# Performance work log

Measured on AMD Instinct MI355X. Metric: run time of the kernel, lower is better.

The kernel has to match this reference:

```python
import jax, jax.numpy as jnp
import numpy as np

EMBED = 1024
HEADS = 16
HEAD_DIM = EMBED // HEADS


def setup_inputs() -> dict:
    key = jax.random.key(0)
    ks = jax.random.split(key, 6)
    scale = 1.0 / np.sqrt(EMBED)
    x = jax.random.normal(ks[0], (2, 2048, EMBED), dtype=jnp.float32)
    # nn.Linear weights stored as [out_features, in_features]
    Wq = jax.random.normal(ks[1], (EMBED, EMBED), dtype=jnp.float32) * scale
    Wk = jax.random.normal(ks[2], (EMBED, EMBED), dtype=jnp.float32) * scale
    Wv = jax.random.normal(ks[3], (EMBED, EMBED), dtype=jnp.float32) * scale
    Wo = jax.random.normal(ks[4], (EMBED, EMBED), dtype=jnp.float32) * scale
    bo = jax.random.normal(ks[5], (EMBED,), dtype=jnp.float32) * scale
    return {"x": x, "Wq": Wq, "Wk": Wk, "Wv": Wv, "Wo": Wo, "bo": bo}


def reference(x, Wq, Wk, Wv, Wo, bo):
    N, L, E = x.shape
    # projections (torch Linear: x @ W.T)
    q = (x @ Wq.T).reshape(N, L, HEADS, HEAD_DIM).transpose(0, 2, 1, 3)  # [N,H,L,D]
    k = (x @ Wk.T).reshape(N, L, HEADS, HEAD_DIM).transpose(0, 2, 1, 3)
    v = (x @ Wv.T).reshape(N, L, HEADS, HEAD_DIM).transpose(0, 2, 1, 3)
    # scores scaled by sqrt(embed_size) (as in source, not sqrt(head_dim))
    scores = jnp.einsum("nhqd,nhkd->nhqk", q, k) / jnp.sqrt(jnp.float32(E))
    attn = jax.nn.softmax(scores, axis=-1)
    out = jnp.einsum("nhqk,nhkd->nhqd", attn, v)  # [N,H,L,D]
    out = out.transpose(0, 2, 1, 3).reshape(N, L, E)
    return out @ Wo.T + bo
```

## Files before the change

### kernel.cpp

```cpp
#include <hip/hip_runtime.h>
#include <hip/hip_bf16.h>

constexpr int NB  = 2;
constexpr int SL  = 2048;
constexpr int EMB = 1024;
constexpr int NH  = 16;
constexpr int HD  = 64;
constexpr int MT  = NB * SL;
constexpr size_t PROJ = (size_t)MT * EMB;

typedef __attribute__((ext_vector_type(8))) short bf16x8;
typedef __attribute__((ext_vector_type(4))) float f32x4;

__device__ inline short f2b(float f) {
  __hip_bfloat16 b = __float2bfloat16(f);
  short s; __builtin_memcpy(&s, &b, 2); return s;
}

#define GLDS16(g, l)                                                     \
  __builtin_amdgcn_global_load_lds(                                      \
      (const __attribute__((address_space(1))) void*)(g),                \
      (__attribute__((address_space(3))) void*)(l), 16, 0, 0)

__global__ __launch_bounds__(256) void cast_all(
    const float* __restrict__ x,  const float* __restrict__ wq,
    const float* __restrict__ wk, const float* __restrict__ wv,
    const float* __restrict__ wo, short* __restrict__ xb,
    short* __restrict__ wqkv, short* __restrict__ wob) {
  const size_t t = (size_t)blockIdx.x * 256 + threadIdx.x;
  const float* src; short* dst; size_t base;
  if (t < 1048576)      { src = x;  dst = xb;              base = 0; }
  else if (t < 1310720) { src = wq; dst = wqkv;            base = 1048576; }
  else if (t < 1572864) { src = wk; dst = wqkv + (1 << 20); base = 1310720; }
  else if (t < 1835008) { src = wv; dst = wqkv + (2 << 20); base = 1572864; }
  else                  { src = wo; dst = wob;             base = 1835008; }
  const size_t i = t - base;
  const float4 v = ((const float4*)src)[i];
  const short4 o = {f2b(v.x), f2b(v.y), f2b(v.z), f2b(v.w)};
  ((short4*)dst)[i] = o;
}

__global__ __launch_bounds__(256) void gemm_qkv(
    const short* __restrict__ A, const short* __restrict__ W,
    short* __restrict__ qb, short* __restrict__ kb, short* __restrict__ vt) {
  __shared__ short As[128 * 32];
  __shared__ short Bs[128 * 32];
  const int tid = threadIdx.x;
  const int w = tid >> 6, lane = tid & 63;
  const int la = lane >> 4, lb = lane & 15;
  const int wm = w & 1, wn = w >> 1;
  const int m0 = blockIdx.y << 7, n0 = blockIdx.x << 7;
  const int srow = lane >> 2, scol = (lane & 3) << 3;
  const short* a0 = A + (size_t)(m0 + w * 16 + srow) * 1024 + scol;
  const short* b0 = W + (size_t)(n0 + w * 16 + srow) * 1024 + scol;
  short* lA0 = As + (w * 16) * 32;
  short* lA1 = As + (64 + w * 16) * 32;
  short* lB0 = Bs + (w * 16) * 32;
  short* lB1 = Bs + (64 + w * 16) * 32;

  f32x4 acc[4][4];
#pragma unroll
  for (int i = 0; i < 4; ++i)
#pragma unroll
    for (int j = 0; j < 4; ++j) acc[i][j] = (f32x4){0.f, 0.f, 0.f, 0.f};

  for (int k0 = 0; k0 < 1024; k0 += 32) {
    __syncthreads();
    GLDS16(a0 + k0, lA0);
    GLDS16(a0 + 64 * 1024 + k0, lA1);
    GLDS16(b0 + k0, lB0);
    GLDS16(b0 + 64 * 1024 + k0, lB1);
    __syncthreads();
    bf16x8 af[4], bf[4];
#pragma unroll
    for (int i = 0; i < 4; ++i)
      af[i] = *(const bf16x8*)&As[(wm * 64 + i * 16 + lb) * 32 + la * 8];
#pragma unroll
    for (int j = 0; j < 4; ++j)
      bf[j] = *(const bf16x8*)&Bs[(wn * 64 + j * 16 + lb) * 32 + la * 8];
#pragma unroll
    for (int i = 0; i < 4; ++i)
#pragma unroll
      for (int j = 0; j < 4; ++j)
        acc[i][j] = __builtin_amdgcn_mfma_f32_16x16x32_bf16(af[i], bf[j],
                                                            acc[i][j], 0, 0, 0);
  }

  const int region = n0 >> 10;
  if (region < 2) {
    short* dst = region ? kb : qb;
    const float sc = region ? 1.0f : 0.03125f * 1.44269504f;
    const int nb0 = n0 & 1023;
#pragma unroll
    for (int j = 0; j < 4; ++j) {
      const int nj = nb0 + wn * 64 + j * 16 + lb;
#pragma unroll
      for (int i = 0; i < 4; ++i) {
        const int mi = m0 + wm * 64 + i * 16 + la * 4;
#pragma unroll
        for (int r = 0; r < 4; ++r)
          dst[(size_t)(mi + r) * 1024 + nj] = f2b(acc[i][j][r] * sc);
      }
    }
  } else {
#pragma unroll
    for (int j = 0; j < 4; ++j) {
      const int nv = (n0 - 2048) + wn * 64 + j * 16 + lb;
      const int h = nv >> 6, d = nv & 63;
#pragma unroll
      for (int i = 0; i < 4; ++i) {
        const int mi = m0 + wm * 64 + i * 16 + la * 4;
        const int nbi = mi >> 11, seq = mi & (SL - 1);
        const int k5 = seq & 31;
        const int seqp = (seq & ~31) | (8 * ((k5 >> 2) & 3) + 4 * (k5 >> 4));
        const short4 o = {f2b(acc[i][j][0]), f2b(acc[i][j][1]),
                          f2b(acc[i][j][2]), f2b(acc[i][j][3])};
        *(short4*)&vt[((size_t)(nbi * NH + h) * HD + d) * SL + seqp] = o;
      }
    }
  }
}

__global__ __launch_bounds__(256) void gemm_out(
    const short* __restrict__ A, const short* __restrict__ W,
    const float* __restrict__ bias, float* __restrict__ out) {
  __shared__ short As[128 * 32];
  __shared__ short Bs[64 * 32];
  const int tid = threadIdx.x;
  const int w = tid >> 6, lane = tid & 63;
  const int la = lane >> 4, lb = lane & 15;
  const int wm = w & 1, wn = w >> 1;
  const int m0 = blockIdx.y << 7, n0 = blockIdx.x << 6;
  const int srow = lane >> 2, scol = (lane & 3) << 3;
  const short* a0 = A + (size_t)(m0 + w * 16 + srow) * 1024 + scol;
  const short* b0 = W + (size_t)(n0 + w * 16 + srow) * 1024 + scol;
  short* lA0 = As + (w * 16) * 32;
  short* lA1 = As + (64 + w * 16) * 32;
  short* lB0 = Bs + (w * 16) * 32;

  f32x4 acc[4][2];
#pragma unroll
  for (int i = 0; i < 4; ++i)
#pragma unroll
    for (int j = 0; j < 2; ++j) acc[i][j] = (f32x4){0.f, 0.f, 0.f, 0.f};

  for (int k0 = 0; k0 < 1024; k0 += 32) {
    __syncthreads();
    GLDS16(a0 + k0, lA0);
    GLDS16(a0 + 64 * 1024 + k0, lA1);
    GLDS16(b0 + k0, lB0);
    __syncthreads();
    bf16x8 af[4], bf[2];
#pragma unroll
    for (int i = 0; i < 4; ++i)
      af[i] = *(const bf16x8*)&As[(wm * 64 + i * 16 + lb) * 32 + la * 8];
#pragma unroll
    for (int j = 0; j < 2; ++j)
      bf[j] = *(const bf16x8*)&Bs[(wn * 32 + j * 16 + lb) * 32 + la * 8];
#pragma unroll
    for (int i = 0; i < 4; ++i)
#pragma unroll
      for (int j = 0; j < 2; ++j)
        acc[i][j] = __builtin_amdgcn_mfma_f32_16x16x32_bf16(af[i], bf[j],
                                                            acc[i][j], 0, 0, 0);
  }
#pragma unroll
  for (int j = 0; j < 2; ++j) {
    const int nj = n0 + wn * 32 + j * 16 + lb;
    const float bv = bias[nj];
#pragma unroll
    for (int i = 0; i < 4; ++i) {
      const int mi = m0 + wm * 64 + i * 16 + la * 4;
#pragma unroll
      for (int r = 0; r < 4; ++r)
        out[(size_t)(mi + r) * 1024 + nj] = acc[i][j][r] + bv;
    }
  }
}

__global__ __launch_bounds__(256, 2) void attn_mfma(const short* __restrict__ Qg,
                                                    const short* __restrict__ Kg,
                                                    const short* __restrict__ Vtg,
                                                    short* __restrict__ Ab) {
  __shared__ __align__(16) short mem[17408];
  __shared__ float lred[128];
  const int tid = threadIdx.x;
  const int w = tid >> 6, lane = tid & 63;
  const int G = lane >> 4, lb = lane & 15;
  const int wk = w & 1, wq = w >> 1;
  const int qt = blockIdx.x, h = blockIdx.y, n = blockIdx.z;

  const bool isK = (w < 2);
  const short* gbase = isK ? (Kg + ((size_t)(n * SL)) * EMB + h * HD)
                           : (Vtg + ((size_t)(n * NH + h)) * HD * SL);
  const size_t gstep = isK ? (size_t)64 * EMB : (size_t)64;
  size_t go[4];
#pragma unroll
  for (int i = 0; i < 4; ++i) {
    if (isK) {
      go[i] = (size_t)(16 * (2 * w + (i >> 1)) + lb) * EMB + 32 * (i & 1) + 8 * G;
    } else {
      go[i] = (size_t)(16 * (2 * (w - 2) + (i >> 1)) + lb) * SL + 32 * (i & 1) + 8 * G;
    }
  }

  const short* Qb = Qg + ((size_t)(n * SL + (qt << 7) + 64 * wq)) * EMB + h * HD;
  bf16x8 bQ[4][2];
#pragma unroll
  for (int nt = 0; nt < 4; ++nt)
#pragma unroll
    for (int ks = 0; ks < 2; ++ks)
      bQ[nt][ks] = *(const bf16x8*)(Qb + (size_t)(16 * nt + lb) * EMB + 32 * ks + 8 * G);

#pragma unroll
  for (int i = 0; i < 4; ++i) GLDS16(gbase + go[i], &mem[(4 * w + i) * 512]);

  f32x4 O[4][4];
  float lacc[4] = {0.f, 0.f, 0.f, 0.f};
#pragma unroll
  for (int i = 0; i < 4; ++i)
#pragma unroll
    for (int j = 0; j < 4; ++j) O[i][j] = (f32x4){0.f, 0.f, 0.f, 0.f};

  for (int kt = 0; kt < SL / 64; ++kt) {
    __syncthreads();
    if (kt + 1 < SL / 64) {
      const short* g = gbase + (size_t)(kt + 1) * gstep;
      const int b = (kt + 1) & 1;
#pragma unroll
      for (int i = 0; i < 4; ++i)
        GLDS16(g + go[i], &mem[(b * 16 + 4 * w + i) * 512]);
    }
    const int c = (kt & 1) * 8192;

    f32x4 S[2][4];
#pragma unroll
    for (int mt = 0; mt < 2; ++mt)
#pragma unroll
      for (int nt = 0; nt < 4; ++nt) S[mt][nt] = (f32x4){0.f, 0.f, 0.f, 0.f};
#pragma unroll
    for (int ks = 0; ks < 2; ++ks) {
      const bf16x8 aK0 = *(const bf16x8*)&mem[c + (4 * wk + ks) * 512 + lane * 8];
      const bf16x8 aK1 = *(const bf16x8*)&mem[c + (4 * wk + 2 + ks) * 512 + lane * 8];
#pragma unroll
      for (int nt = 0; nt < 4; ++nt) {
        S[0][nt] = __builtin_amdgcn_mfma_f32_16x16x32_bf16(aK0, bQ[nt][ks],
                                                           S[0][nt], 0, 0, 0);
        S[1][nt] = __builtin_amdgcn_mfma_f32_16x16x32_bf16(aK1, bQ[nt][ks],
                                                           S[1][nt], 0, 0, 0);
      }
    }

#pragma unroll
    for (int nt = 0; nt < 4; ++nt)
#pragma unroll
      for (int mt = 0; mt < 2; ++mt)
#pragma unroll
        for (int r = 0; r < 4; ++r) {
          const float p = __builtin_amdgcn_exp2f(S[mt][nt][r]);
          S[mt][nt][r] = p;
          lacc[nt] += p;
        }

    bf16x8 aV[4];
#pragma unroll
    for (int mtd = 0; mtd < 4; ++mtd)
      aV[mtd] = *(const bf16x8*)&mem[c + (8 + 2 * mtd + wk) * 512 + lane * 8];
#pragma unroll
    for (int nt = 0; nt < 4; ++nt) {
      bf16x8 B2;
      B2[0] = f2b(S[0][nt][0]);
      B2[1] = f2b(S[0][nt][1]);
      B2[2] = f2b(S[0][nt][2]);
      B2[3] = f2b(S[0][nt][3]);
      B2[4] = f2b(S[1][nt][0]);
      B2[5] = f2b(S[1][nt][1]);
      B2[6] = f2b(S[1][nt][2]);
      B2[7] = f2b(S[1][nt][3]);
#pragma unroll
      for (int mtd = 0; mtd < 4; ++mtd)
        O[mtd][nt] = __builtin_amdgcn_mfma_f32_16x16x32_bf16(aV[mtd], B2,
                                                             O[mtd][nt], 0, 0, 0);
    }
  }

#pragma unroll
  for (int nt = 0; nt < 4; ++nt) {
    lacc[nt] += __shfl_xor(lacc[nt], 16);
    lacc[nt] += __shfl_xor(lacc[nt], 32);
  }

  float* red = (float*)mem;
  __syncthreads();
  if (wk == 1) {
#pragma unroll
    for (int nt = 0; nt < 4; ++nt) {
      const int q = 16 * nt + lb;
#pragma unroll
      for (int mtd = 0; mtd < 4; ++mtd)
        *(f32x4*)&red[wq * 4352 + q * 68 + 16 * mtd + 4 * G] = O[mtd][nt];
      if (G == 0) lred[wq * 64 + q] = lacc[nt];
    }
  }
  __syncthreads();
  if (wk == 0) {
    short* Ao = Ab + ((size_t)(n * SL + (qt << 7) + 64 * wq)) * EMB + h * HD;
#pragma unroll
    for (int nt = 0; nt < 4; ++nt) {
      const int q = 16 * nt + lb;
      const float inv = 1.f / (lacc[nt] + lred[wq * 64 + q]);
#pragma unroll
      for (int mtd = 0; mtd < 4; ++mtd) {
        const f32x4 t = *(const f32x4*)&red[wq * 4352 + q * 68 + 16 * mtd + 4 * G];
        const f32x4 s = t + O[mtd][nt];
        const short4 o = {f2b(s[0] * inv), f2b(s[1] * inv), f2b(s[2] * inv),
                          f2b(s[3] * inv)};
        *(short4*)(Ao + (size_t)q * EMB + 16 * mtd + 4 * G) = o;
      }
    }
  }
}

extern "C" void kernel_launch(void* const* d_in, const int* in_sizes, int n_in,
                              void* d_out, int out_size, void* d_ws, size_t ws_size,
                              hipStream_t stream) {
  const float* x  = (const float*)d_in[0];
  const float* Wq = (const float*)d_in[1];
  const float* Wk = (const float*)d_in[2];
  const float* Wv = (const float*)d_in[3];
  const float* Wo = (const float*)d_in[4];
  const float* bo = (const float*)d_in[5];
  float* out = (float*)d_out;

  short* xb   = (short*)d_ws;
  short* wqkv = xb + PROJ;
  short* wob  = wqkv + 3u * EMB * EMB;
  short* qb   = wob + (size_t)EMB * EMB;
  short* kb   = qb + PROJ;
  short* vt   = kb + PROJ;
  short* ab   = qb;

  cast_all<<<8192, 256, 0, stream>>>(x, Wq, Wk, Wv, Wo, xb, wqkv, wob);
  gemm_qkv<<<dim3(24, 32), 256, 0, stream>>>(xb, wqkv, qb, kb, vt);
  attn_mfma<<<dim3(SL / 128, NH, NB), 256, 0, stream>>>(qb, kb, vt, ab);
  gemm_out<<<dim3(16, 32), 256, 0, stream>>>(ab, wob, bo, out);
}
```

Baseline: 186.5 us.

## Replace async global-to-LDS double buffer with register-prefetched single padded LDS tile

```diff
diff --git a/kernel.cpp b/kernel.cpp
--- a/kernel.cpp
+++ b/kernel.cpp
@@ -182,27 +182,17 @@
                                                     const short* __restrict__ Kg,
                                                     const short* __restrict__ Vtg,
                                                     short* __restrict__ Ab) {
-  __shared__ __align__(16) short mem[17408];
+  __shared__ __align__(16) char smem[34816];
   __shared__ float lred[128];
+  short (*Ks)[72] = (short(*)[72])smem;
+  short (*Vt)[72] = (short(*)[72])(smem + 64 * 72 * 2);
+  float* red = (float*)smem;
   const int tid = threadIdx.x;
   const int w = tid >> 6, lane = tid & 63;
   const int G = lane >> 4, lb = lane & 15;
   const int wk = w & 1, wq = w >> 1;
   const int qt = blockIdx.x, h = blockIdx.y, n = blockIdx.z;
-
-  const bool isK = (w < 2);
-  const short* gbase = isK ? (Kg + ((size_t)(n * SL)) * EMB + h * HD)
-                           : (Vtg + ((size_t)(n * NH + h)) * HD * SL);
-  const size_t gstep = isK ? (size_t)64 * EMB : (size_t)64;
-  size_t go[4];
-#pragma unroll
-  for (int i = 0; i < 4; ++i) {
-    if (isK) {
-      go[i] = (size_t)(16 * (2 * w + (i >> 1)) + lb) * EMB + 32 * (i & 1) + 8 * G;
-    } else {
-      go[i] = (size_t)(16 * (2 * (w - 2) + (i >> 1)) + lb) * SL + 32 * (i & 1) + 8 * G;
-    }
-  }
+  const int row = tid >> 3, c = (tid & 7) << 3;
 
   const short* Qb = Qg + ((size_t)(n * SL + (qt << 7) + 64 * wq)) * EMB + h * HD;
   bf16x8 bQ[4][2];
@@ -210,10 +200,8 @@
   for (int nt = 0; nt < 4; ++nt)
 #pragma unroll
     for (int ks = 0; ks < 2; ++ks)
-      bQ[nt][ks] = *(const bf16x8*)(Qb + (size_t)(16 * nt + lb) * EMB + 32 * ks + 8 * G);
-
-#pragma unroll
-  for (int i = 0; i < 4; ++i) GLDS16(gbase + go[i], &mem[(4 * w + i) * 512]);
+      bQ[nt][ks] =
+          *(const bf16x8*)(Qb + (size_t)(16 * nt + lb) * EMB + 32 * ks + 8 * G);
 
   f32x4 O[4][4];
   float lacc[4] = {0.f, 0.f, 0.f, 0.f};
@@ -222,16 +210,33 @@
 #pragma unroll
     for (int j = 0; j < 4; ++j) O[i][j] = (f32x4){0.f, 0.f, 0.f, 0.f};
 
+  const short* Kb0 = Kg + ((size_t)(n * SL)) * EMB + h * HD;
+  const short* Vb0 = Vtg + ((size_t)(n * NH + h)) * HD * SL;
+
+  bf16x8 pk[2], pv[2];
+#pragma unroll
+  for (int k = 0; k < 2; ++k) {
+    pk[k] = *(const bf16x8*)(Kb0 + (size_t)(row + 32 * k) * EMB + c);
+    pv[k] = *(const bf16x8*)(Vb0 + (size_t)(row + 32 * k) * SL + c);
+  }
+
   for (int kt = 0; kt < SL / 64; ++kt) {
     __syncthreads();
+#pragma unroll
+    for (int k = 0; k < 2; ++k) {
+      *(bf16x8*)&Ks[row + 32 * k][c] = pk[k];
+      *(bf16x8*)&Vt[row + 32 * k][c] = pv[k];
+    }
+    __syncthreads();
     if (kt + 1 < SL / 64) {
-      const short* g = gbase + (size_t)(kt + 1) * gstep;
-      const int b = (kt + 1) & 1;
-#pragma unroll
-      for (int i = 0; i < 4; ++i)
-        GLDS16(g + go[i], &mem[(b * 16 + 4 * w + i) * 512]);
-    }
-    const int c = (kt & 1) * 8192;
+      const short* Kb = Kb0 + (size_t)(kt + 1) * 64 * EMB;
+      const short* Vb = Vb0 + (size_t)(kt + 1) * 64;
+#pragma unroll
+      for (int k = 0; k < 2; ++k) {
+        pk[k] = *(const bf16x8*)(Kb + (size_t)(row + 32 * k) * EMB + c);
+        pv[k] = *(const bf16x8*)(Vb + (size_t)(row + 32 * k) * SL + c);
+      }
+    }
 
     f32x4 S[2][4];
 #pragma unroll
@@ -240,8 +245,8 @@
       for (int nt = 0; nt < 4; ++nt) S[mt][nt] = (f32x4){0.f, 0.f, 0.f, 0.f};
 #pragma unroll
     for (int ks = 0; ks < 2; ++ks) {
-      const bf16x8 aK0 = *(const bf16x8*)&mem[c + (4 * wk + ks) * 512 + lane * 8];
-      const bf16x8 aK1 = *(const bf16x8*)&mem[c + (4 * wk + 2 + ks) * 512 + lane * 8];
+      const bf16x8 aK0 = *(const bf16x8*)&Ks[32 * wk + lb][32 * ks + 8 * G];
+      const bf16x8 aK1 = *(const bf16x8*)&Ks[32 * wk + 16 + lb][32 * ks + 8 * G];
 #pragma unroll
       for (int nt = 0; nt < 4; ++nt) {
         S[0][nt] = __builtin_amdgcn_mfma_f32_16x16x32_bf16(aK0, bQ[nt][ks],
@@ -265,7 +270,7 @@
     bf16x8 aV[4];
 #pragma unroll
     for (int mtd = 0; mtd < 4; ++mtd)
-      aV[mtd] = *(const bf16x8*)&mem[c + (8 + 2 * mtd + wk) * 512 + lane * 8];
+      aV[mtd] = *(const bf16x8*)&Vt[16 * mtd + lb][32 * wk + 8 * G];
 #pragma unroll
     for (int nt = 0; nt < 4; ++nt) {
       bf16x8 B2;
@@ -290,7 +295,6 @@
     lacc[nt] += __shfl_xor(lacc[nt], 32);
   }
 
-  float* red = (float*)mem;
   __syncthreads();
   if (wk == 1) {
 #pragma unroll
```

Result: faster. 178.9 us (-4.1%).
